# Performance work log

Hardware: AMD Instinct MI355X
Metric: run time of the kernel (lower is better)

## Reference

```python
import jax, jax.numpy as jnp
import numpy as np

D = 256          # volume side
N_LABELS = 1000  # number of distinct vessel IDs (0 = background)


def setup_inputs() -> dict:
    key = jax.random.key(0)
    k1, k2, k3, k4 = jax.random.split(key, 4)
    vessel_labels = jax.random.randint(k1, (D, D, D), 0, N_LABELS, dtype=jnp.int32)
    keep_mask = jax.random.randint(k2, (N_LABELS,), 0, 2, dtype=jnp.int32)
    # per-label intensity in [0, 0.7) or [1.3, 2) depending on a coin flip,
    # matching sample_label_intensity's Uniform(0,0.7) / Uniform(1.3,2)
    u = jax.random.uniform(k3, (N_LABELS,))
    coin = jax.random.bernoulli(k4, 0.5, (N_LABELS,))
    intensity_lut = jnp.where(coin, 1.3 + 0.7 * u, 0.7 * u).astype(jnp.float32)
    parenchyma = jax.random.uniform(jax.random.fold_in(key, 9), (D, D, D), dtype=jnp.float32)
    return {
        "vessel_labels": vessel_labels,
        "keep_mask": keep_mask,
        "intensity_lut": intensity_lut,
        "parenchyma": parenchyma,
    }


def reference(vessel_labels, keep_mask, intensity_lut, parenchyma):
    # prune_labels: hide labels whose keep_mask is 0 (set them to background 0)
    keep = keep_mask[vessel_labels] > 0          # [D,D,D] bool, single gather
    labels = jnp.where(keep, vessel_labels, 0)   # pruned label volume

    # sample_label_intensity as a LUT gather: O(voxels) instead of
    # O(labels * voxels) masked_fill_ loop. Background (label 0) -> 1.0.
    lut = intensity_lut.at[0].set(jnp.float32(1.0))
    vessel_intensities = lut[labels]             # [D,D,D] float32

    # vessel mask = labels.clip(0, 1).to(int16)
    vessel_mask = (labels > 0).astype(jnp.int16)

    # parenchyma[mask>0] *= intensities[mask>0]
    out = parenchyma * jnp.where(vessel_mask > 0, vessel_intensities, jnp.float32(1.0))
    return out, vessel_mask
```

## Files before the change

kernel.cpp:

```cpp
#include <hip/hip_runtime.h>

#define DVOL 256
#define NVOX (DVOL * DVOL * DVOL)
#define N_LABELS 1000

#define BLOCK   256
#define NGROUPS (NVOX / 4)
#define NBLOCKS (NGROUPS / BLOCK)

typedef float f32x4 __attribute__((ext_vector_type(4)));
typedef int   i32x4 __attribute__((ext_vector_type(4)));

__global__ __launch_bounds__(BLOCK)
void build_fused_lut(const int* __restrict__ keep_mask,
                     const float* __restrict__ intensity_lut,
                     float* __restrict__ fused)
{
    for (int l = threadIdx.x; l < N_LABELS; l += BLOCK) {
        const bool keep = (l > 0) && (keep_mask[l] > 0);
        fused[l] = keep ? intensity_lut[l] : 1.0f;
    }
}

__global__ __launch_bounds__(BLOCK)
void vessel_fuse_kernel(const int* __restrict__ labels,
                        const float* __restrict__ fused,
                        const float* __restrict__ parenchyma,
                        float* __restrict__ out,
                        float* __restrict__ maskf)
{
    const int i = blockIdx.x * BLOCK + threadIdx.x;

    const i32x4 L = __builtin_nontemporal_load((const i32x4*)labels + i);
    const f32x4 P = __builtin_nontemporal_load((const f32x4*)parenchyma + i);

    f32x4 s;
    s.x = fused[L.x];
    s.y = fused[L.y];
    s.z = fused[L.z];
    s.w = fused[L.w];

    f32x4 o, m;
    o.x = P.x * s.x;  m.x = (s.x != 1.0f) ? 1.0f : 0.0f;
    o.y = P.y * s.y;  m.y = (s.y != 1.0f) ? 1.0f : 0.0f;
    o.z = P.z * s.z;  m.z = (s.z != 1.0f) ? 1.0f : 0.0f;
    o.w = P.w * s.w;  m.w = (s.w != 1.0f) ? 1.0f : 0.0f;

    __builtin_nontemporal_store(o, (f32x4*)out + i);
    __builtin_nontemporal_store(m, (f32x4*)maskf + i);
}

__global__ __launch_bounds__(BLOCK)
void vessel_fuse_lds(const int* __restrict__ labels,
                     const int* __restrict__ keep_mask,
                     const float* __restrict__ intensity_lut,
                     const float* __restrict__ parenchyma,
                     float* __restrict__ out,
                     float* __restrict__ maskf)
{
    __shared__ float s_scale[N_LABELS];
    for (int l = threadIdx.x; l < N_LABELS; l += BLOCK) {
        const bool keep = (l > 0) && (keep_mask[l] > 0);
        s_scale[l] = keep ? intensity_lut[l] : 1.0f;
    }
    __syncthreads();

    const i32x4* lab4 = (const i32x4*)labels;
    const f32x4* par4 = (const f32x4*)parenchyma;
    f32x4* out4 = (f32x4*)out;
    f32x4* msk4 = (f32x4*)maskf;

    const int stride = gridDim.x * blockDim.x;
    for (int i = blockIdx.x * BLOCK + threadIdx.x; i < NGROUPS; i += stride) {
        const i32x4 L = lab4[i];
        const f32x4 P = par4[i];
        f32x4 s, o, m;
        s.x = s_scale[L.x]; s.y = s_scale[L.y];
        s.z = s_scale[L.z]; s.w = s_scale[L.w];
        o.x = P.x * s.x;  m.x = (s.x != 1.0f) ? 1.0f : 0.0f;
        o.y = P.y * s.y;  m.y = (s.y != 1.0f) ? 1.0f : 0.0f;
        o.z = P.z * s.z;  m.z = (s.z != 1.0f) ? 1.0f : 0.0f;
        o.w = P.w * s.w;  m.w = (s.w != 1.0f) ? 1.0f : 0.0f;
        out4[i] = o;
        msk4[i] = m;
    }
}

extern "C" void kernel_launch(void* const* d_in, const int* in_sizes, int n_in,
                              void* d_out, int out_size, void* d_ws, size_t ws_size,
                              hipStream_t stream) {
    (void)in_sizes; (void)n_in; (void)out_size;

    const int*   vessel_labels = (const int*)d_in[0];
    const int*   keep_mask     = (const int*)d_in[1];
    const float* intensity_lut = (const float*)d_in[2];
    const float* parenchyma    = (const float*)d_in[3];

    float* out   = (float*)d_out;
    float* maskf = (float*)d_out + NVOX;

    if (d_ws != nullptr && ws_size >= N_LABELS * sizeof(float)) {
        float* fused = (float*)d_ws;
        build_fused_lut<<<1, BLOCK, 0, stream>>>(keep_mask, intensity_lut, fused);
        vessel_fuse_kernel<<<NBLOCKS, BLOCK, 0, stream>>>(
            vessel_labels, fused, parenchyma, out, maskf);
    } else {
        vessel_fuse_lds<<<4096, BLOCK, 0, stream>>>(
            vessel_labels, keep_mask, intensity_lut, parenchyma, out, maskf);
    }
}
```

Before: 230.4 us.

## Split fused kernel into separate mask and output kernels with per-thread loops

Splits the single fused gather kernel into a mask-writing kernel and an output-writing kernel, each processing several vec4 groups per thread over a fixed 2048-block grid. The label volume (64 MiB) is now read twice, once per kernel, and an extra launch is added; the second read may partly hit in cache. The split likely aims to reduce per-kernel register and memory-stream pressure, at the cost of extra DRAM traffic. Labels are now read with normal instead of nontemporal loads.

Measured after the change: 251.4 us. 9.1% more time.

```diff
diff --git a/kernel.cpp b/kernel.cpp
--- a/kernel.cpp
+++ b/kernel.cpp
@@ -6,7 +6,9 @@
 
 #define BLOCK   256
 #define NGROUPS (NVOX / 4)
-#define NBLOCKS (NGROUPS / BLOCK)
+#define NBLOCKS 2048
+#define GPB     (NGROUPS / NBLOCKS)
+#define KITER   (GPB / BLOCK)
 
 typedef float f32x4 __attribute__((ext_vector_type(4)));
 typedef int   i32x4 __attribute__((ext_vector_type(4)));
@@ -23,31 +25,50 @@
 }
 
 __global__ __launch_bounds__(BLOCK)
-void vessel_fuse_kernel(const int* __restrict__ labels,
-                        const float* __restrict__ fused,
-                        const float* __restrict__ parenchyma,
-                        float* __restrict__ out,
-                        float* __restrict__ maskf)
+void mask_kernel(const int* __restrict__ labels,
+                 const float* __restrict__ fused,
+                 float* __restrict__ maskf)
 {
-    const int i = blockIdx.x * BLOCK + threadIdx.x;
+    const int base = blockIdx.x * GPB + threadIdx.x;
+    const i32x4* lab4 = (const i32x4*)labels;
+    f32x4* msk4 = (f32x4*)maskf;
 
-    const i32x4 L = __builtin_nontemporal_load((const i32x4*)labels + i);
-    const f32x4 P = __builtin_nontemporal_load((const f32x4*)parenchyma + i);
+#pragma unroll
+    for (int k = 0; k < KITER; ++k) {
+        const int i = base + k * BLOCK;
+        const i32x4 L = lab4[i];
+        f32x4 m;
+        m.x = (fused[L.x] != 1.0f) ? 1.0f : 0.0f;
+        m.y = (fused[L.y] != 1.0f) ? 1.0f : 0.0f;
+        m.z = (fused[L.z] != 1.0f) ? 1.0f : 0.0f;
+        m.w = (fused[L.w] != 1.0f) ? 1.0f : 0.0f;
+        __builtin_nontemporal_store(m, msk4 + i);
+    }
+}
 
-    f32x4 s;
-    s.x = fused[L.x];
-    s.y = fused[L.y];
-    s.z = fused[L.z];
-    s.w = fused[L.w];
+__global__ __launch_bounds__(BLOCK)
+void out_kernel(const int* __restrict__ labels,
+                const float* __restrict__ fused,
+                const float* __restrict__ parenchyma,
+                float* __restrict__ out)
+{
+    const int base = blockIdx.x * GPB + threadIdx.x;
+    const i32x4* lab4 = (const i32x4*)labels;
+    const f32x4* par4 = (const f32x4*)parenchyma;
+    f32x4* out4 = (f32x4*)out;
 
-    f32x4 o, m;
-    o.x = P.x * s.x;  m.x = (s.x != 1.0f) ? 1.0f : 0.0f;
-    o.y = P.y * s.y;  m.y = (s.y != 1.0f) ? 1.0f : 0.0f;
-    o.z = P.z * s.z;  m.z = (s.z != 1.0f) ? 1.0f : 0.0f;
-    o.w = P.w * s.w;  m.w = (s.w != 1.0f) ? 1.0f : 0.0f;
-
-    __builtin_nontemporal_store(o, (f32x4*)out + i);
-    __builtin_nontemporal_store(m, (f32x4*)maskf + i);
+#pragma unroll
+    for (int k = 0; k < KITER; ++k) {
+        const int i = base + k * BLOCK;
+        const i32x4 L = lab4[i];
+        const f32x4 P = __builtin_nontemporal_load(par4 + i);
+        f32x4 o;
+        o.x = P.x * fused[L.x];
+        o.y = P.y * fused[L.y];
+        o.z = P.z * fused[L.z];
+        o.w = P.w * fused[L.w];
+        __builtin_nontemporal_store(o, out4 + i);
+    }
 }
 
 __global__ __launch_bounds__(BLOCK)
@@ -102,8 +123,9 @@
     if (d_ws != nullptr && ws_size >= N_LABELS * sizeof(float)) {
         float* fused = (float*)d_ws;
         build_fused_lut<<<1, BLOCK, 0, stream>>>(keep_mask, intensity_lut, fused);
-        vessel_fuse_kernel<<<NBLOCKS, BLOCK, 0, stream>>>(
-            vessel_labels, fused, parenchyma, out, maskf);
+        mask_kernel<<<NBLOCKS, BLOCK, 0, stream>>>(vessel_labels, fused, maskf);
+        out_kernel<<<NBLOCKS, BLOCK, 0, stream>>>(vessel_labels, fused,
+                                                  parenchyma, out);
     } else {
         vessel_fuse_lds<<<4096, BLOCK, 0, stream>>>(
             vessel_labels, keep_mask, intensity_lut, parenchyma, out, maskf);
```
